# Performance work log

Hardware: AMD Instinct MI355X
Metric: run time of the kernel (lower is better)

## Reference

```python
import jax, jax.numpy as jnp
import numpy as np

N_HEAD = 16
D_HEAD = 64
D_MODEL = 1024
QLEN = 1024
BSZ = 4
RLEN = 1024
CONV = 7
SCALE = 1.0 / D_HEAD ** 0.5
NEG = -1e30
EPS = 1e-5


def setup_inputs() -> dict:
    key = jax.random.key(0)
    ks = jax.random.split(key, 14)
    s = 0.02
    inp = {
        "w": jax.random.normal(ks[0], (QLEN, BSZ, D_MODEL), jnp.float32),
        "r": jax.random.normal(ks[1], (RLEN, D_MODEL), jnp.float32),
        "r_w_bias": jax.random.normal(ks[2], (N_HEAD, D_HEAD), jnp.float32) * s,
        "r_r_bias": jax.random.normal(ks[3], (N_HEAD, D_HEAD), jnp.float32) * s,
        "W_qkv": jax.random.normal(ks[4], (3 * N_HEAD * D_HEAD, D_MODEL), jnp.float32) * s,
        "W_r": jax.random.normal(ks[5], (N_HEAD * D_HEAD, D_MODEL), jnp.float32) * s,
        "W_o": jax.random.normal(ks[6], (D_MODEL, N_HEAD * D_HEAD), jnp.float32) * s,
        "conv_wq": jax.random.normal(ks[7], (D_HEAD, D_HEAD, CONV), jnp.float32) * s,
        "conv_bq": jax.random.normal(ks[8], (D_HEAD,), jnp.float32) * s,
        "conv_wk": jax.random.normal(ks[9], (D_HEAD, D_HEAD, CONV), jnp.float32) * s,
        "conv_bk": jax.random.normal(ks[10], (D_HEAD,), jnp.float32) * s,
        "conv_wv": jax.random.normal(ks[11], (D_HEAD, D_HEAD, CONV), jnp.float32) * s,
        "conv_bv": jax.random.normal(ks[12], (D_HEAD,), jnp.float32) * s,
        "ln_gamma": jnp.ones((D_MODEL,), jnp.float32),
        "ln_beta": jnp.zeros((D_MODEL,), jnp.float32),
        # causal mask, True = masked out (original dim==3 branch: [qlen, klen, 1])
        "attn_mask": jnp.triu(jnp.ones((QLEN, QLEN), bool), k=1)[:, :, None],
    }
    return inp


def _conv1d(x, wgt, b):
    # x: [N, C, L], wgt: [O, I, K] (torch Conv1d layout), same padding
    y = jax.lax.conv_general_dilated(x, wgt, (1,), [(CONV // 2, CONV // 2)],
                                     dimension_numbers=("NCH", "OIH", "NCH"))
    return y + b[None, :, None]


def _rel_shift(x):
    # x: [q, k, b, n] -> Transformer-XL relative shift
    q, k, b, n = x.shape
    xp = jnp.concatenate([jnp.zeros((q, 1, b, n), x.dtype), x], axis=1)
    return xp.reshape(k + 1, q, b, n)[1:].reshape(q, k, b, n)


def reference(w, r, r_w_bias, r_r_bias, W_qkv, W_r, W_o,
              conv_wq, conv_bq, conv_wk, conv_bk, conv_wv, conv_bv,
              ln_gamma, ln_beta, attn_mask):
    qlen, bsz, _ = w.shape
    klen = qlen  # mems=None

    heads = jnp.einsum('qbm,hm->qbh', w, W_qkv)  # [q, b, 3*n*d]
    hq, hk, hv = jnp.split(heads, 3, axis=-1)

    def to_conv(x, L):
        # [L, b, n*d] -> [n*b, d, L]
        return x.reshape(L, bsz, N_HEAD, D_HEAD).transpose(2, 1, 3, 0).reshape(N_HEAD * bsz, D_HEAD, L)

    def from_conv(x, L):
        # [n*b, d, L] -> [L, b, n, d]
        return x.reshape(N_HEAD, bsz, D_HEAD, L).transpose(3, 1, 0, 2)

    q_h = from_conv(_conv1d(to_conv(hq, qlen), conv_wq, conv_bq), qlen)
    k_h = from_conv(_conv1d(to_conv(hk, klen), conv_wk, conv_bk), klen)
    v_h = from_conv(_conv1d(to_conv(hv, klen), conv_wv, conv_bv), klen)

    r_head_k = (r @ W_r.T).reshape(-1, N_HEAD, D_HEAD)  # [rlen, n, d]

    AC = jnp.einsum('ibnd,jbnd->ijbn', q_h + r_w_bias, k_h)
    BD = _rel_shift(jnp.einsum('ibnd,jnd->ijbn', q_h + r_r_bias, r_head_k))
    score = (AC + BD) * SCALE
    score = jnp.where(attn_mask[:, :, :, None], NEG, score)

    prob = jax.nn.softmax(score, axis=1)
    vec = jnp.einsum('ijbn,jbnd->ibnd', prob, v_h).reshape(qlen, bsz, N_HEAD * D_HEAD)
    attn_out = vec @ W_o.T

    x = w + attn_out
    mu = jnp.mean(x, axis=-1, keepdims=True)
    var = jnp.mean(jnp.square(x - mu), axis=-1, keepdims=True)
    return (x - mu) / jnp.sqrt(var + EPS) * ln_gamma + ln_beta
```

## Files before the change

### kernel.cpp

```cpp
#include <hip/hip_runtime.h>
#include <math.h>

#define L 1024
#define SCALEF 0.125f
#define NEGF -1e30f

typedef unsigned short u16;
typedef __bf16 bf16x8 __attribute__((ext_vector_type(8)));
typedef float f32x4 __attribute__((ext_vector_type(4)));
typedef unsigned short u16x8 __attribute__((ext_vector_type(8)));
typedef unsigned short u16x4 __attribute__((ext_vector_type(4)));

#define MFMA(a, b, c) __builtin_amdgcn_mfma_f32_16x16x32_bf16(a, b, c, 0, 0, 0)

__device__ inline u16 f2b(float f) {
  union { float f; unsigned u; } v; v.f = f;
  unsigned r = v.u + 0x7fffu + ((v.u >> 16) & 1u);
  return (u16)(r >> 16);
}

__device__ __forceinline__ void ld16(u16* lds, const u16* g) {
  __builtin_amdgcn_global_load_lds((const __attribute__((address_space(1))) unsigned int*)g,
                                   (__attribute__((address_space(3))) unsigned int*)lds, 16, 0, 0);
}

__global__ __launch_bounds__(256) void prep(const float* __restrict__ w, const float* __restrict__ Wqkv,
                                            const float* __restrict__ r, const float* __restrict__ Wr,
                                            const float* __restrict__ Wo,
                                            const float* __restrict__ cwq, const float* __restrict__ cwk,
                                            const float* __restrict__ cwv,
                                            u16* w_bf, u16* wqkv_bf, u16* r_bf, u16* wr_bf, u16* wo_bf,
                                            u16* wTq, u16* wTk, u16* wTv) {
  int i = blockIdx.x * 256 + threadIdx.x;
  if (i < 2621440) {
    const float* s; u16* d; int off;
    if (i < 1048576)      { s = w;    d = w_bf;    off = i; }
    else if (i < 1835008) { s = Wqkv; d = wqkv_bf; off = i - 1048576; }
    else if (i < 2097152) { s = r;    d = r_bf;    off = i - 1835008; }
    else if (i < 2359296) { s = Wr;   d = wr_bf;   off = i - 2097152; }
    else                  { s = Wo;   d = wo_bf;   off = i - 2359296; }
    float4 v = ((const float4*)s)[off];
    u16x4 o = {f2b(v.x), f2b(v.y), f2b(v.z), f2b(v.w)};
    ((u16x4*)d)[off] = o;
  } else {
    int j = i - 2621440;
    if (j < 86016) {
      int z = j / 28672, rem = j % 28672;
      const float* src = z == 0 ? cwq : z == 1 ? cwk : cwv;
      u16* dst = z == 0 ? wTq : z == 1 ? wTk : wTv;
      int tt = rem >> 12, rem2 = rem & 4095;
      int dout = rem2 >> 6, din = rem2 & 63;
      dst[rem] = f2b(src[(dout * 64 + din) * 7 + tt]);
    }
  }
}

template <int OB>
__device__ __forceinline__ void gemm_tile(u16* sA, u16* sB, const u16* A, const u16* B,
                                          void* Cp, int N, int K, int m0, int n0) {
  int t = threadIdx.x;
  int w = t >> 6, lane = t & 63;
  int q4 = lane >> 4, li = lane & 15;
  int mw = (w & 1) << 6, nw = (w >> 1) << 6;
  f32x4 acc[4][4];
#pragma unroll
  for (int i = 0; i < 4; ++i)
#pragma unroll
    for (int j = 0; j < 4; ++j) acc[i][j] = (f32x4){0.f, 0.f, 0.f, 0.f};
  int r0 = t >> 2, c0 = (t & 3) << 3;
  const u16* Ap0 = A + (size_t)(m0 + r0) * K + c0;
  const u16* Ap1 = A + (size_t)(m0 + 64 + r0) * K + c0;
  const u16* Bp0 = B + (size_t)(n0 + r0) * K + c0;
  const u16* Bp1 = B + (size_t)(n0 + 64 + r0) * K + c0;
  u16* sAw = sA + w * 512;
  u16* sBw = sB + w * 512;
  for (int kb = 0; kb < K; kb += 32) {
    __syncthreads();
    ld16(sAw, Ap0 + kb);
    ld16(sAw + 2048, Ap1 + kb);
    ld16(sBw, Bp0 + kb);
    ld16(sBw + 2048, Bp1 + kb);
    __syncthreads();
    bf16x8 fa[4], fb[4];
#pragma unroll
    for (int i = 0; i < 4; ++i) fa[i] = *(const bf16x8*)&sA[(mw + i * 16 + li) * 32 + q4 * 8];
#pragma unroll
    for (int i = 0; i < 4; ++i) fb[i] = *(const bf16x8*)&sB[(nw + i * 16 + li) * 32 + q4 * 8];
#pragma unroll
    for (int mt = 0; mt < 4; ++mt)
#pragma unroll
      for (int nt = 0; nt < 4; ++nt) acc[mt][nt] = MFMA(fa[mt], fb[nt], acc[mt][nt]);
  }
#pragma unroll
  for (int mt = 0; mt < 4; ++mt)
#pragma unroll
    for (int r = 0; r < 4; ++r) {
      size_t row = m0 + mw + mt * 16 + q4 * 4 + r;
      if (OB) {
        u16* C = (u16*)Cp;
#pragma unroll
        for (int nt = 0; nt < 4; ++nt) C[row * N + n0 + nw + nt * 16 + li] = f2b(acc[mt][nt][r]);
      } else {
        float* C = (float*)Cp;
#pragma unroll
        for (int nt = 0; nt < 4; ++nt) C[row * N + n0 + nw + nt * 16 + li] = acc[mt][nt][r];
      }
    }
}

__global__ __launch_bounds__(256) void gemm_stage1(const u16* __restrict__ w_bf, const u16* __restrict__ wqkv_bf,
                                                   u16* __restrict__ heads,
                                                   const u16* __restrict__ r_bf, const u16* __restrict__ wr_bf,
                                                   u16* __restrict__ rhk) {
  __shared__ u16 sA[128 * 32];
  __shared__ u16 sB[128 * 32];
  int id = blockIdx.x;
  if (id < 768) {
    gemm_tile<1>(sA, sB, w_bf, wqkv_bf, heads, 3072, 1024, (id / 24) << 7, (id % 24) << 7);
  } else {
    int j = id - 768;
    gemm_tile<1>(sA, sB, r_bf, wr_bf, rhk, 1024, 1024, (j >> 3) << 7, (j & 7) << 7);
  }
}

__global__ __launch_bounds__(256) void gemm_wo(const u16* __restrict__ vec, const u16* __restrict__ wo_bf,
                                               float* __restrict__ attnf) {
  __shared__ u16 sA[128 * 32];
  __shared__ u16 sB[128 * 32];
  gemm_tile<0>(sA, sB, vec, wo_bf, attnf, 1024, 1024, (int)(blockIdx.y << 7), (int)(blockIdx.x << 7));
}

__global__ __launch_bounds__(256) void conv3(const u16* __restrict__ x,
                                             const u16* __restrict__ wTq, const u16* __restrict__ wTk,
                                             const u16* __restrict__ wTv,
                                             const float* __restrict__ cbq, const float* __restrict__ cbk,
                                             const float* __restrict__ cbv,
                                             u16* __restrict__ qh, u16* __restrict__ kh, u16* __restrict__ vtg) {
  __shared__ u16 sX[70 * 72];
  int z = blockIdx.z;
  const u16* wT = z == 0 ? wTq : z == 1 ? wTk : wTv;
  const float* bias = z == 0 ? cbq : z == 1 ? cbk : cbv;
  int t = threadIdx.x;
  int w = t >> 6, lane = t & 63;
  int q4 = lane >> 4, li = lane & 15;
  int l0 = blockIdx.x << 6, bn = blockIdx.y;
  int b = bn >> 4, n = bn & 15;
  const u16* xb = x + b * 3072 + z * 1024 + n * 64;
  for (int e = t; e < 560; e += 256) {
    int ro = e >> 3, c = e & 7;
    int l = l0 - 3 + ro;
    u16x8 v = {0, 0, 0, 0, 0, 0, 0, 0};
    if (l >= 0 && l < L) v = *(const u16x8*)(xb + (size_t)l * 12288 + c * 8);
    *(u16x8*)&sX[ro * 72 + c * 8] = v;
  }
  bf16x8 Bw[7][2];
#pragma unroll
  for (int tt = 0; tt < 7; ++tt)
#pragma unroll
    for (int kc = 0; kc < 2; ++kc)
      Bw[tt][kc] = *(const bf16x8*)(wT + (tt * 64 + w * 16 + li) * 64 + kc * 32 + q4 * 8);
  f32x4 acc[4];
#pragma unroll
  for (int i = 0; i < 4; ++i) acc[i] = (f32x4){0.f, 0.f, 0.f, 0.f};
  __syncthreads();
#pragma unroll
  for (int tt = 0; tt < 7; ++tt)
#pragma unroll
    for (int kc = 0; kc < 2; ++kc)
#pragma unroll
      for (int mt = 0; mt < 4; ++mt) {
        bf16x8 a = *(const bf16x8*)&sX[(mt * 16 + li + tt) * 72 + kc * 32 + q4 * 8];
        acc[mt] = MFMA(a, Bw[tt][kc], acc[mt]);
      }
  float bv = bias[w * 16 + li];
  if (z < 2) {
    u16* out = z == 0 ? qh : kh;
#pragma unroll
    for (int mt = 0; mt < 4; ++mt)
#pragma unroll
      for (int r = 0; r < 4; ++r) {
        int l = l0 + mt * 16 + q4 * 4 + r;
        out[(((size_t)l * 4 + b) * 16 + n) * 64 + w * 16 + li] = f2b(acc[mt][r] + bv);
      }
  } else {
    __syncthreads();
#pragma unroll
    for (int mt = 0; mt < 4; ++mt)
#pragma unroll
      for (int r = 0; r < 4; ++r)
        sX[(w * 16 + li) * 72 + mt * 16 + q4 * 4 + r] = f2b(acc[mt][r] + bv);
    __syncthreads();
    int d = t >> 2, ch = t & 3;
    u16x8 v0 = *(u16x8*)&sX[d * 72 + ch * 16];
    u16x8 v1 = *(u16x8*)&sX[d * 72 + ch * 16 + 8];
    u16* dst = vtg + ((size_t)bn * 64 + d) * 1024 + l0 + ch * 16;
    *(u16x8*)dst = v0;
    *(u16x8*)(dst + 8) = v1;
  }
}

__global__ __launch_bounds__(256) void rel_attn(const u16* __restrict__ qh, const u16* __restrict__ kh,
                                                const u16* __restrict__ vt, const u16* __restrict__ rhk,
                                                const float* __restrict__ rwb_, const float* __restrict__ rrb_,
                                                u16* __restrict__ vec) {
  __shared__ u16 sK[64][72];
  __shared__ u16 sVt[64][72];
  __shared__ u16 sR[128][72];
  __shared__ u16 sP[4][16][72];
  int t = threadIdx.x;
  int w = t >> 6, lane = t & 63;
  int q4 = lane >> 4, li = lane & 15;
  int p = blockIdx.x, bn = blockIdx.y;
  int b = bn >> 4, n = bn & 15;
  float rwbv[2][8], rrbv[2][8];
#pragma unroll
  for (int kc = 0; kc < 2; ++kc)
#pragma unroll
    for (int j = 0; j < 8; ++j) {
      int d = kc * 32 + q4 * 8 + j;
      rwbv[kc][j] = rwb_[n * 64 + d];
      rrbv[kc][j] = rrb_[n * 64 + d];
    }
  int base_w = 48 - w * 16;
  const u16* vtb = vt + (size_t)bn * 64 * 1024;
  for (int half = 0; half < 2; ++half) {
    int qt = (half == 0) ? p : 15 - p;
    int i0 = qt << 6;
    bf16x8 Aw[2], Ar[2];
    {
      const u16* qrow = qh + (((size_t)(i0 + w * 16 + li) * 4 + b) * 16 + n) * 64;
#pragma unroll
      for (int kc = 0; kc < 2; ++kc) {
        bf16x8 qv = *(const bf16x8*)(qrow + kc * 32 + q4 * 8);
        bf16x8 aw, ar;
#pragma unroll
        for (int j = 0; j < 8; ++j) {
          float qf = (float)qv[j];
          aw[j] = (__bf16)(qf + rwbv[kc][j]);
          ar[j] = (__bf16)(qf + rrbv[kc][j]);
        }
        Aw[kc] = aw;
        Ar[kc] = ar;
      }
    }
    f32x4 accO[4];
#pragma unroll
    for (int i = 0; i < 4; ++i) accO[i] = (f32x4){0.f, 0.f, 0.f, 0.f};
    float mst[4], lst[4];
#pragma unroll
    for (int r = 0; r < 4; ++r) { mst[r] = -INFINITY; lst[r] = 0.f; }
    int ntile = qt + 1;
    for (int jt = 0; jt < ntile; ++jt) {
      int j0 = jt << 6;
      int gB = 960 - i0 + j0;
      for (int e = t; e < 512; e += 256) {
        int row = e >> 3, c = e & 7;
        *(u16x8*)&sK[row][c * 8] =
            *(const u16x8*)(kh + (((size_t)(j0 + row) * 4 + b) * 16 + n) * 64 + c * 8);
      }
      for (int e = t; e < 512; e += 256) {
        int d = e >> 3, c = e & 7;
        *(u16x8*)&sVt[d][c * 8] = *(const u16x8*)(vtb + (size_t)d * 1024 + j0 + c * 8);
      }
      for (int e = t; e < 1024; e += 256) {
        int m = e >> 3, c = e & 7;
        int g = gB + m;
        if (g > L - 1) g = L - 1;
        *(u16x8*)&sR[m][c * 8] = *(const u16x8*)(rhk + (size_t)g * 1024 + n * 64 + c * 8);
      }
      __syncthreads();
      f32x4 accS[4], accG[5];
#pragma unroll
      for (int i = 0; i < 4; ++i) accS[i] = (f32x4){0.f, 0.f, 0.f, 0.f};
#pragma unroll
      for (int i = 0; i < 5; ++i) accG[i] = (f32x4){0.f, 0.f, 0.f, 0.f};
#pragma unroll
      for (int kc = 0; kc < 2; ++kc) {
#pragma unroll
        for (int nt = 0; nt < 4; ++nt) {
          bf16x8 fk = *(const bf16x8*)&sK[nt * 16 + li][kc * 32 + q4 * 8];
          accS[nt] = MFMA(Aw[kc], fk, accS[nt]);
        }
#pragma unroll
        for (int nt = 0; nt < 5; ++nt) {
          bf16x8 fr = *(const bf16x8*)&sR[base_w + nt * 16 + li][kc * 32 + q4 * 8];
          accG[nt] = MFMA(Ar[kc], fr, accG[nt]);
        }
      }
      float Sv[4][4];
#pragma unroll
      for (int nt = 0; nt < 4; ++nt)
#pragma unroll
        for (int r = 0; r < 4; ++r) {
          int il = q4 * 4 + r;
          int srcc = li + 15 - il;
          int lsrc = (lane & 48) | (srcc & 15);
          float g0 = __shfl(accG[nt][r], lsrc);
          float g1 = __shfl(accG[nt + 1][r], lsrc);
          float g = (srcc < 16) ? g0 : g1;
          float s = (accS[nt][r] + g) * SCALEF;
          if (j0 + nt * 16 + li > i0 + w * 16 + il) s = NEGF;
          Sv[nt][r] = s;
        }
      float mnew[4], alpha[4], psum[4];
#pragma unroll
      for (int r = 0; r < 4; ++r) {
        float mx = fmaxf(fmaxf(Sv[0][r], Sv[1][r]), fmaxf(Sv[2][r], Sv[3][r]));
        mx = fmaxf(mx, __shfl_xor(mx, 1));
        mx = fmaxf(mx, __shfl_xor(mx, 2));
        mx = fmaxf(mx, __shfl_xor(mx, 4));
        mx = fmaxf(mx, __shfl_xor(mx, 8));
        mnew[r] = fmaxf(mst[r], mx);
        alpha[r] = __expf(mst[r] - mnew[r]);
        psum[r] = 0.f;
      }
#pragma unroll
      for (int nt = 0; nt < 4; ++nt)
#pragma unroll
        for (int r = 0; r < 4; ++r) {
          float pv = __expf(Sv[nt][r] - mnew[r]);
          psum[r] += pv;
          sP[w][q4 * 4 + r][nt * 16 + li] = f2b(pv);
        }
#pragma unroll
      for (int r = 0; r < 4; ++r) {
        float ps = psum[r];
        ps += __shfl_xor(ps, 1);
        ps += __shfl_xor(ps, 2);
        ps += __shfl_xor(ps, 4);
        ps += __shfl_xor(ps, 8);
        lst[r] = lst[r] * alpha[r] + ps;
        mst[r] = mnew[r];
      }
#pragma unroll
      for (int nt = 0; nt < 4; ++nt) {
        f32x4 o = accO[nt];
#pragma unroll
        for (int r = 0; r < 4; ++r) o[r] *= alpha[r];
        accO[nt] = o;
      }
#pragma unroll
      for (int kc = 0; kc < 2; ++kc) {
        bf16x8 ap = *(const bf16x8*)&sP[w][li][kc * 32 + q4 * 8];
#pragma unroll
        for (int nt = 0; nt < 4; ++nt) {
          bf16x8 fv = *(const bf16x8*)&sVt[nt * 16 + li][kc * 32 + q4 * 8];
          accO[nt] = MFMA(ap, fv, accO[nt]);
        }
      }
      __syncthreads();
    }
#pragma unroll
    for (int r = 0; r < 4; ++r) {
      int il = q4 * 4 + r;
      int ig = i0 + w * 16 + il;
      float inv = 1.0f / lst[r];
      u16* orow = vec + (((size_t)ig * 4 + b) * 16 + n) * 64;
#pragma unroll
      for (int nt = 0; nt < 4; ++nt) orow[nt * 16 + li] = f2b(accO[nt][r] * inv);
    }
  }
}

__global__ __launch_bounds__(256) void resid_ln(const float* __restrict__ w,
                                                const float* __restrict__ attn,
                                                const float* __restrict__ gamma,
                                                const float* __restrict__ beta,
                                                float* __restrict__ out) {
  __shared__ float ssum[4], ssq[4];
  int row = blockIdx.x, t = threadIdx.x;
  float4 xw = *(const float4*)&w[(size_t)row * 1024 + t * 4];
  float4 xa = *(const float4*)&attn[(size_t)row * 1024 + t * 4];
  float4 x = make_float4(xw.x + xa.x, xw.y + xa.y, xw.z + xa.z, xw.w + xa.w);
  float s = x.x + x.y + x.z + x.w;
  float sq = x.x * x.x + x.y * x.y + x.z * x.z + x.w * x.w;
#pragma unroll
  for (int off = 32; off > 0; off >>= 1) {
    s += __shfl_down(s, off);
    sq += __shfl_down(sq, off);
  }
  int wid = t >> 6;
  if ((t & 63) == 0) { ssum[wid] = s; ssq[wid] = sq; }
  __syncthreads();
  s = ssum[0] + ssum[1] + ssum[2] + ssum[3];
  sq = ssq[0] + ssq[1] + ssq[2] + ssq[3];
  float mean = s * (1.0f / 1024.0f);
  float var = sq * (1.0f / 1024.0f) - mean * mean;
  float rstd = rsqrtf(var + 1e-5f);
  float4 g = *(const float4*)&gamma[t * 4];
  float4 bb = *(const float4*)&beta[t * 4];
  float4 o;
  o.x = (x.x - mean) * rstd * g.x + bb.x;
  o.y = (x.y - mean) * rstd * g.y + bb.y;
  o.z = (x.z - mean) * rstd * g.z + bb.z;
  o.w = (x.w - mean) * rstd * g.w + bb.w;
  *(float4*)&out[(size_t)row * 1024 + t * 4] = o;
}

extern "C" void kernel_launch(void* const* d_in, const int* in_sizes, int n_in,
                              void* d_out, int out_size, void* d_ws, size_t ws_size,
                              hipStream_t stream) {
  const float* w     = (const float*)d_in[0];
  const float* r     = (const float*)d_in[1];
  const float* rwb   = (const float*)d_in[2];
  const float* rrb   = (const float*)d_in[3];
  const float* W_qkv = (const float*)d_in[4];
  const float* W_r   = (const float*)d_in[5];
  const float* W_o   = (const float*)d_in[6];
  const float* cwq   = (const float*)d_in[7];
  const float* cbq   = (const float*)d_in[8];
  const float* cwk   = (const float*)d_in[9];
  const float* cbk   = (const float*)d_in[10];
  const float* cwv   = (const float*)d_in[11];
  const float* cbv   = (const float*)d_in[12];
  const float* gamma = (const float*)d_in[13];
  const float* beta  = (const float*)d_in[14];
  float* outp = (float*)d_out;

  char* wsb = (char*)d_ws;
  u16*   heads   = (u16*)(wsb);
  u16*   vec     = (u16*)(wsb);
  float* attnf   = (float*)(wsb + 8388608);
  u16*   qh      = (u16*)(wsb + 25165824);
  u16*   kh      = (u16*)(wsb + 33554432);
  u16*   rhk     = (u16*)(wsb + 50331648);
  u16*   w_bf    = (u16*)(wsb + 52428800);
  u16*   wqkv_bf = (u16*)(wsb + 60817408);
  u16*   r_bf    = (u16*)(wsb + 67108864);
  u16*   wr_bf   = (u16*)(wsb + 69206016);
  u16*   wo_bf   = (u16*)(wsb + 71303168);
  u16*   wTq     = (u16*)(wsb + 73400320);
  u16*   wTk     = (u16*)(wsb + 73457664);
  u16*   wTv     = (u16*)(wsb + 73515008);
  u16*   vt      = (u16*)(wsb + 73572352);

  dim3 blk(256);
  prep<<<10576, blk, 0, stream>>>(w, W_qkv, r, W_r, W_o, cwq, cwk, cwv,
                                  w_bf, wqkv_bf, r_bf, wr_bf, wo_bf, wTq, wTk, wTv);
  gemm_stage1<<<832, blk, 0, stream>>>(w_bf, wqkv_bf, heads, r_bf, wr_bf, rhk);
  conv3<<<dim3(16, 64, 3), blk, 0, stream>>>(heads, wTq, wTk, wTv, cbq, cbk, cbv, qh, kh, vt);
  rel_attn<<<dim3(8, 64), blk, 0, stream>>>(qh, kh, vt, rhk, rwb, rrb, vec);
  gemm_wo<<<dim3(8, 32), blk, 0, stream>>>(vec, wo_bf, attnf);
  resid_ln<<<4096, blk, 0, stream>>>(w, attnf, gamma, beta, outp);
}
```

Baseline: 311.3 us.

## Split attention into one query tile per block and shrink Wo GEMM tiles

```diff
diff --git a/kernel.cpp b/kernel.cpp
--- a/kernel.cpp
+++ b/kernel.cpp
@@ -123,11 +123,51 @@
   }
 }
 
-__global__ __launch_bounds__(256) void gemm_wo(const u16* __restrict__ vec, const u16* __restrict__ wo_bf,
-                                               float* __restrict__ attnf) {
-  __shared__ u16 sA[128 * 32];
+__global__ __launch_bounds__(256) void gemm_wo(const u16* __restrict__ A, const u16* __restrict__ B,
+                                               float* __restrict__ C) {
+  __shared__ u16 sA[64 * 32];
   __shared__ u16 sB[128 * 32];
-  gemm_tile<0>(sA, sB, vec, wo_bf, attnf, 1024, 1024, (int)(blockIdx.y << 7), (int)(blockIdx.x << 7));
+  int t = threadIdx.x;
+  int w = t >> 6, lane = t & 63;
+  int q4 = lane >> 4, li = lane & 15;
+  int m0 = blockIdx.y << 6, n0 = blockIdx.x << 7;
+  int nw = w << 5;
+  const int N = 1024, K = 1024;
+  f32x4 acc[4][2];
+#pragma unroll
+  for (int i = 0; i < 4; ++i)
+#pragma unroll
+    for (int j = 0; j < 2; ++j) acc[i][j] = (f32x4){0.f, 0.f, 0.f, 0.f};
+  int r0 = t >> 2, c0 = (t & 3) << 3;
+  const u16* Ap = A + (size_t)(m0 + r0) * K + c0;
+  const u16* Bp0 = B + (size_t)(n0 + r0) * K + c0;
+  const u16* Bp1 = B + (size_t)(n0 + 64 + r0) * K + c0;
+  u16* sAw = sA + w * 512;
+  u16* sBw = sB + w * 512;
+  for (int kb = 0; kb < K; kb += 32) {
+    __syncthreads();
+    ld16(sAw, Ap + kb);
+    ld16(sBw, Bp0 + kb);
+    ld16(sBw + 2048, Bp1 + kb);
+    __syncthreads();
+    bf16x8 fa[4], fb[2];
+#pragma unroll
+    for (int i = 0; i < 4; ++i) fa[i] = *(const bf16x8*)&sA[(i * 16 + li) * 32 + q4 * 8];
+#pragma unroll
+    for (int j = 0; j < 2; ++j) fb[j] = *(const bf16x8*)&sB[(nw + j * 16 + li) * 32 + q4 * 8];
+#pragma unroll
+    for (int mt = 0; mt < 4; ++mt)
+#pragma unroll
+      for (int nt = 0; nt < 2; ++nt) acc[mt][nt] = MFMA(fa[mt], fb[nt], acc[mt][nt]);
+  }
+#pragma unroll
+  for (int mt = 0; mt < 4; ++mt)
+#pragma unroll
+    for (int r = 0; r < 4; ++r) {
+      size_t row = m0 + mt * 16 + q4 * 4 + r;
+#pragma unroll
+      for (int nt = 0; nt < 2; ++nt) C[row * N + n0 + nw + nt * 16 + li] = acc[mt][nt][r];
+    }
 }
 
 __global__ __launch_bounds__(256) void conv3(const u16* __restrict__ x,
@@ -199,10 +239,10 @@
   }
 }
 
-__global__ __launch_bounds__(256) void rel_attn(const u16* __restrict__ qh, const u16* __restrict__ kh,
-                                                const u16* __restrict__ vt, const u16* __restrict__ rhk,
-                                                const float* __restrict__ rwb_, const float* __restrict__ rrb_,
-                                                u16* __restrict__ vec) {
+__global__ __launch_bounds__(256, 3) void rel_attn(const u16* __restrict__ qh, const u16* __restrict__ kh,
+                                                   const u16* __restrict__ vt, const u16* __restrict__ rhk,
+                                                   const float* __restrict__ rwb_, const float* __restrict__ rrb_,
+                                                   u16* __restrict__ vec) {
   __shared__ u16 sK[64][72];
   __shared__ u16 sVt[64][72];
   __shared__ u16 sR[128][72];
@@ -210,155 +250,149 @@
   int t = threadIdx.x;
   int w = t >> 6, lane = t & 63;
   int q4 = lane >> 4, li = lane & 15;
-  int p = blockIdx.x, bn = blockIdx.y;
+  int qt = 15 - blockIdx.x, bn = blockIdx.y;
   int b = bn >> 4, n = bn & 15;
-  float rwbv[2][8], rrbv[2][8];
-#pragma unroll
-  for (int kc = 0; kc < 2; ++kc)
-#pragma unroll
-    for (int j = 0; j < 8; ++j) {
-      int d = kc * 32 + q4 * 8 + j;
-      rwbv[kc][j] = rwb_[n * 64 + d];
-      rrbv[kc][j] = rrb_[n * 64 + d];
-    }
   int base_w = 48 - w * 16;
   const u16* vtb = vt + (size_t)bn * 64 * 1024;
-  for (int half = 0; half < 2; ++half) {
-    int qt = (half == 0) ? p : 15 - p;
-    int i0 = qt << 6;
-    bf16x8 Aw[2], Ar[2];
-    {
-      const u16* qrow = qh + (((size_t)(i0 + w * 16 + li) * 4 + b) * 16 + n) * 64;
-#pragma unroll
-      for (int kc = 0; kc < 2; ++kc) {
-        bf16x8 qv = *(const bf16x8*)(qrow + kc * 32 + q4 * 8);
-        bf16x8 aw, ar;
-#pragma unroll
-        for (int j = 0; j < 8; ++j) {
-          float qf = (float)qv[j];
-          aw[j] = (__bf16)(qf + rwbv[kc][j]);
-          ar[j] = (__bf16)(qf + rrbv[kc][j]);
-        }
-        Aw[kc] = aw;
-        Ar[kc] = ar;
-      }
-    }
-    f32x4 accO[4];
-#pragma unroll
-    for (int i = 0; i < 4; ++i) accO[i] = (f32x4){0.f, 0.f, 0.f, 0.f};
-    float mst[4], lst[4];
-#pragma unroll
-    for (int r = 0; r < 4; ++r) { mst[r] = -INFINITY; lst[r] = 0.f; }
-    int ntile = qt + 1;
-    for (int jt = 0; jt < ntile; ++jt) {
-      int j0 = jt << 6;
-      int gB = 960 - i0 + j0;
-      for (int e = t; e < 512; e += 256) {
-        int row = e >> 3, c = e & 7;
-        *(u16x8*)&sK[row][c * 8] =
-            *(const u16x8*)(kh + (((size_t)(j0 + row) * 4 + b) * 16 + n) * 64 + c * 8);
-      }
-      for (int e = t; e < 512; e += 256) {
-        int d = e >> 3, c = e & 7;
-        *(u16x8*)&sVt[d][c * 8] = *(const u16x8*)(vtb + (size_t)d * 1024 + j0 + c * 8);
-      }
-      for (int e = t; e < 1024; e += 256) {
-        int m = e >> 3, c = e & 7;
-        int g = gB + m;
-        if (g > L - 1) g = L - 1;
-        *(u16x8*)&sR[m][c * 8] = *(const u16x8*)(rhk + (size_t)g * 1024 + n * 64 + c * 8);
-      }
-      __syncthreads();
-      f32x4 accS[4], accG[5];
-#pragma unroll
-      for (int i = 0; i < 4; ++i) accS[i] = (f32x4){0.f, 0.f, 0.f, 0.f};
-#pragma unroll
-      for (int i = 0; i < 5; ++i) accG[i] = (f32x4){0.f, 0.f, 0.f, 0.f};
-#pragma unroll
-      for (int kc = 0; kc < 2; ++kc) {
-#pragma unroll
-        for (int nt = 0; nt < 4; ++nt) {
-          bf16x8 fk = *(const bf16x8*)&sK[nt * 16 + li][kc * 32 + q4 * 8];
-          accS[nt] = MFMA(Aw[kc], fk, accS[nt]);
-        }
-#pragma unroll
-        for (int nt = 0; nt < 5; ++nt) {
-          bf16x8 fr = *(const bf16x8*)&sR[base_w + nt * 16 + li][kc * 32 + q4 * 8];
-          accG[nt] = MFMA(Ar[kc], fr, accG[nt]);
-        }
-      }
-      float Sv[4][4];
+  int i0 = qt << 6;
+  bf16x8 Aw[2], Ar[2];
+  {
+    const u16* qrow = qh + (((size_t)(i0 + w * 16 + li) * 4 + b) * 16 + n) * 64;
+#pragma unroll
+    for (int kc = 0; kc < 2; ++kc) {
+      bf16x8 qv = *(const bf16x8*)(qrow + kc * 32 + q4 * 8);
+      bf16x8 aw, ar;
+#pragma unroll
+      for (int j = 0; j < 8; ++j) {
+        int d = kc * 32 + q4 * 8 + j;
+        float qf = (float)qv[j];
+        aw[j] = (__bf16)(qf + rwb_[n * 64 + d]);
+        ar[j] = (__bf16)(qf + rrb_[n * 64 + d]);
+      }
+      Aw[kc] = aw;
+      Ar[kc] = ar;
+    }
+  }
+  f32x4 accO[4];
+#pragma unroll
+  for (int i = 0; i < 4; ++i) accO[i] = (f32x4){0.f, 0.f, 0.f, 0.f};
+  float mst[4], lst[4];
+#pragma unroll
+  for (int r = 0; r < 4; ++r) { mst[r] = -INFINITY; lst[r] = 0.f; }
+  int ntile = qt + 1;
+  for (int jt = 0; jt < ntile; ++jt) {
+    int j0 = jt << 6;
+    int gB = 960 - i0 + j0;
+    for (int e = t; e < 512; e += 256) {
+      int row = e >> 3, c = e & 7;
+      *(u16x8*)&sK[row][c * 8] =
+          *(const u16x8*)(kh + (((size_t)(j0 + row) * 4 + b) * 16 + n) * 64 + c * 8);
+    }
+    for (int e = t; e < 512; e += 256) {
+      int d = e >> 3, c = e & 7;
+      *(u16x8*)&sVt[d][c * 8] = *(const u16x8*)(vtb + (size_t)d * 1024 + j0 + c * 8);
+    }
+    for (int e = t; e < 1024; e += 256) {
+      int m = e >> 3, c = e & 7;
+      int g = gB + m;
+      if (g > L - 1) g = L - 1;
+      *(u16x8*)&sR[m][c * 8] = *(const u16x8*)(rhk + (size_t)g * 1024 + n * 64 + c * 8);
+    }
+    __syncthreads();
+    f32x4 accS[4], accG[5];
+#pragma unroll
+    for (int i = 0; i < 4; ++i) accS[i] = (f32x4){0.f, 0.f, 0.f, 0.f};
+#pragma unroll
+    for (int i = 0; i < 5; ++i) accG[i] = (f32x4){0.f, 0.f, 0.f, 0.f};
+#pragma unroll
+    for (int kc = 0; kc < 2; ++kc) {
+#pragma unroll
+      for (int nt = 0; nt < 4; ++nt) {
+        bf16x8 fk = *(const bf16x8*)&sK[nt * 16 + li][kc * 32 + q4 * 8];
+        accS[nt] = MFMA(Aw[kc], fk, accS[nt]);
+      }
+#pragma unroll
+      for (int nt = 0; nt < 5; ++nt) {
+        bf16x8 fr = *(const bf16x8*)&sR[base_w + nt * 16 + li][kc * 32 + q4 * 8];
+        accG[nt] = MFMA(Ar[kc], fr, accG[nt]);
+      }
+    }
+    float Sv[4][4];
+#pragma unroll
+    for (int nt = 0; nt < 4; ++nt)
+#pragma unroll
+      for (int r = 0; r < 4; ++r) {
+        int il = q4 * 4 + r;
+        int srcc = li + 15 - il;
+        int lsrc = (lane & 48) | (srcc & 15);
+        float g0 = __shfl(accG[nt][r], lsrc);
+        float g1 = __shfl(accG[nt + 1][r], lsrc);
+        float g = (srcc < 16) ? g0 : g1;
+        Sv[nt][r] = (accS[nt][r] + g) * SCALEF;
+      }
+    if (jt == qt) {
 #pragma unroll
       for (int nt = 0; nt < 4; ++nt)
 #pragma unroll
-        for (int r = 0; r < 4; ++r) {
-          int il = q4 * 4 + r;
-          int srcc = li + 15 - il;
-          int lsrc = (lane & 48) | (srcc & 15);
-          float g0 = __shfl(accG[nt][r], lsrc);
-          float g1 = __shfl(accG[nt + 1][r], lsrc);
-          float g = (srcc < 16) ? g0 : g1;
-          float s = (accS[nt][r] + g) * SCALEF;
-          if (j0 + nt * 16 + li > i0 + w * 16 + il) s = NEGF;
-          Sv[nt][r] = s;
-        }
-      float mnew[4], alpha[4], psum[4];
+        for (int r = 0; r < 4; ++r)
+          if (j0 + nt * 16 + li > i0 + w * 16 + q4 * 4 + r) Sv[nt][r] = NEGF;
+    }
+    float mnew[4], alpha[4], psum[4];
+#pragma unroll
+    for (int r = 0; r < 4; ++r) {
+      float mx = fmaxf(fmaxf(Sv[0][r], Sv[1][r]), fmaxf(Sv[2][r], Sv[3][r]));
+      mx = fmaxf(mx, __shfl_xor(mx, 1));
+      mx = fmaxf(mx, __shfl_xor(mx, 2));
+      mx = fmaxf(mx, __shfl_xor(mx, 4));
+      mx = fmaxf(mx, __shfl_xor(mx, 8));
+      mnew[r] = fmaxf(mst[r], mx);
+      alpha[r] = __expf(mst[r] - mnew[r]);
+      psum[r] = 0.f;
+    }
+#pragma unroll
+    for (int nt = 0; nt < 4; ++nt)
 #pragma unroll
       for (int r = 0; r < 4; ++r) {
-        float mx = fmaxf(fmaxf(Sv[0][r], Sv[1][r]), fmaxf(Sv[2][r], Sv[3][r]));
-        mx = fmaxf(mx, __shfl_xor(mx, 1));
-        mx = fmaxf(mx, __shfl_xor(mx, 2));
-        mx = fmaxf(mx, __shfl_xor(mx, 4));
-        mx = fmaxf(mx, __shfl_xor(mx, 8));
-        mnew[r] = fmaxf(mst[r], mx);
-        alpha[r] = __expf(mst[r] - mnew[r]);
-        psum[r] = 0.f;
-      }
-#pragma unroll
-      for (int nt = 0; nt < 4; ++nt)
-#pragma unroll
-        for (int r = 0; r < 4; ++r) {
-          float pv = __expf(Sv[nt][r] - mnew[r]);
-          psum[r] += pv;
-          sP[w][q4 * 4 + r][nt * 16 + li] = f2b(pv);
-        }
-#pragma unroll
-      for (int r = 0; r < 4; ++r) {
-        float ps = psum[r];
-        ps += __shfl_xor(ps, 1);
-        ps += __shfl_xor(ps, 2);
-        ps += __shfl_xor(ps, 4);
-        ps += __shfl_xor(ps, 8);
-        lst[r] = lst[r] * alpha[r] + ps;
-        mst[r] = mnew[r];
-      }
+        float pv = __expf(Sv[nt][r] - mnew[r]);
+        psum[r] += pv;
+        sP[w][q4 * 4 + r][nt * 16 + li] = f2b(pv);
+      }
+#pragma unroll
+    for (int r = 0; r < 4; ++r) {
+      float ps = psum[r];
+      ps += __shfl_xor(ps, 1);
+      ps += __shfl_xor(ps, 2);
+      ps += __shfl_xor(ps, 4);
+      ps += __shfl_xor(ps, 8);
+      lst[r] = lst[r] * alpha[r] + ps;
+      mst[r] = mnew[r];
+    }
+#pragma unroll
+    for (int nt = 0; nt < 4; ++nt) {
+      f32x4 o = accO[nt];
+#pragma unroll
+      for (int r = 0; r < 4; ++r) o[r] *= alpha[r];
+      accO[nt] = o;
+    }
+#pragma unroll
+    for (int kc = 0; kc < 2; ++kc) {
+      bf16x8 ap = *(const bf16x8*)&sP[w][li][kc * 32 + q4 * 8];
 #pragma unroll
       for (int nt = 0; nt < 4; ++nt) {
-        f32x4 o = accO[nt];
-#pragma unroll
-        for (int r = 0; r < 4; ++r) o[r] *= alpha[r];
-        accO[nt] = o;
-      }
-#pragma unroll
-      for (int kc = 0; kc < 2; ++kc) {
-        bf16x8 ap = *(const bf16x8*)&sP[w][li][kc * 32 + q4 * 8];
-#pragma unroll
-        for (int nt = 0; nt < 4; ++nt) {
-          bf16x8 fv = *(const bf16x8*)&sVt[nt * 16 + li][kc * 32 + q4 * 8];
-          accO[nt] = MFMA(ap, fv, accO[nt]);
-        }
-      }
-      __syncthreads();
-    }
-#pragma unroll
-    for (int r = 0; r < 4; ++r) {
-      int il = q4 * 4 + r;
-      int ig = i0 + w * 16 + il;
-      float inv = 1.0f / lst[r];
-      u16* orow = vec + (((size_t)ig * 4 + b) * 16 + n) * 64;
-#pragma unroll
-      for (int nt = 0; nt < 4; ++nt) orow[nt * 16 + li] = f2b(accO[nt][r] * inv);
-    }
+        bf16x8 fv = *(const bf16x8*)&sVt[nt * 16 + li][kc * 32 + q4 * 8];
+        accO[nt] = MFMA(ap, fv, accO[nt]);
+      }
+    }
+    __syncthreads();
+  }
+#pragma unroll
+  for (int r = 0; r < 4; ++r) {
+    int il = q4 * 4 + r;
+    int ig = i0 + w * 16 + il;
+    float inv = 1.0f / lst[r];
+    u16* orow = vec + (((size_t)ig * 4 + b) * 16 + n) * 64;
+#pragma unroll
+    for (int nt = 0; nt < 4; ++nt) orow[nt * 16 + li] = f2b(accO[nt][r] * inv);
   }
 }
 
@@ -439,7 +473,7 @@
                                   w_bf, wqkv_bf, r_bf, wr_bf, wo_bf, wTq, wTk, wTv);
   gemm_stage1<<<832, blk, 0, stream>>>(w_bf, wqkv_bf, heads, r_bf, wr_bf, rhk);
   conv3<<<dim3(16, 64, 3), blk, 0, stream>>>(heads, wTq, wTk, wTv, cbq, cbk, cbv, qh, kh, vt);
-  rel_attn<<<dim3(8, 64), blk, 0, stream>>>(qh, kh, vt, rhk, rwb, rrb, vec);
-  gemm_wo<<<dim3(8, 32), blk, 0, stream>>>(vec, wo_bf, attnf);
+  rel_attn<<<dim3(16, 64), blk, 0, stream>>>(qh, kh, vt, rhk, rwb, rrb, vec);
+  gemm_wo<<<dim3(8, 64), blk, 0, stream>>>(vec, wo_bf, attnf);
   resid_ln<<<4096, blk, 0, stream>>>(w, attnf, gamma, beta, outp);
 }
```

Result: slower. 379.7 us (+22.0%).
